# Optimization experiments

Measured on AMD Instinct MI355X. Metric: run time of the kernel, lower is better.

Reference implementation:

```python
import jax, jax.numpy as jnp
import numpy as np

B, N, X, Y, W1, W2, D = 2, 6, 8, 8, 8, 8, 128
H, DH = 4, 32
L = X * Y          # number of windows
QT = N * W1 * W2   # tokens per window
EPS = 1e-5


def _ln(x, g, b):
    m = x.mean(-1, keepdims=True)
    v = ((x - m) ** 2).mean(-1, keepdims=True)
    return (x - m) * jax.lax.rsqrt(v + EPS) * g + b


def _win(t):
    # b n x y w1 w2 d -> b (x y) (n w1 w2) d
    return t.transpose(0, 2, 3, 1, 4, 5, 6).reshape(B, L, QT, D)


def setup_inputs() -> dict:
    key = jax.random.key(0)
    ks = jax.random.split(key, 12)
    s = 0.02
    inp = {
        'q': jax.random.normal(ks[0], (B, N, X, Y, W1, W2, D), jnp.float32),
        'k': jax.random.normal(ks[1], (B, N, X, Y, W1, W2, D), jnp.float32),
        'v': jax.random.normal(ks[2], (B, N, X, Y, W1, W2, D), jnp.float32),
        'skip': jax.random.normal(ks[3], (B, X, Y, W1, W2, D), jnp.float32),
        'gq': jnp.ones((D,), jnp.float32), 'betq': jnp.zeros((D,), jnp.float32),
        'gk': jnp.ones((D,), jnp.float32), 'betk': jnp.zeros((D,), jnp.float32),
        'gv': jnp.ones((D,), jnp.float32), 'betv': jnp.zeros((D,), jnp.float32),
        'wq': jax.random.normal(ks[4], (D, H * DH), jnp.float32) * s,
        'bq': jnp.zeros((H * DH,), jnp.float32),
        'wk': jax.random.normal(ks[5], (D, H * DH), jnp.float32) * s,
        'bk': jnp.zeros((H * DH,), jnp.float32),
        'wv': jax.random.normal(ks[6], (D, H * DH), jnp.float32) * s,
        'bv': jnp.zeros((H * DH,), jnp.float32),
        'wp': jax.random.normal(ks[7], (H * DH, D), jnp.float32) * s,
        'bp': jnp.zeros((D,), jnp.float32),
    }
    return inp


def reference(q, k, v, skip, gq, betq, gk, betk, gv, betv,
              wq, bq, wk, bk, wv, bv, wp, bp):
    scale = DH ** -0.5
    qw, kw, vw = _win(q), _win(k), _win(v)
    # LayerNorm + Linear QKV, split heads: (b, l, T, h, dh)
    qh = (_ln(qw, gq, betq) @ wq + bq).reshape(B, L, QT, H, DH)
    kh = (_ln(kw, gk, betk) @ wk + bk).reshape(B, L, QT, H, DH)
    vh = (_ln(vw, gv, betv) @ wv + bv).reshape(B, L, QT, H, DH)
    dot = scale * jnp.einsum('blqhd,blkhd->bhlqk', qh, kh)
    att = jax.nn.softmax(dot, axis=-1)
    a = jnp.einsum('bhlqk,blkhd->blqhd', att, vh).reshape(B, L, QT, H * DH)
    # b (x y) (n w1 w2) d -> b n x y w1 w2 d
    a = a.reshape(B, X, Y, N, W1, W2, H * DH).transpose(0, 3, 1, 2, 4, 5, 6)
    z = a @ wp + bp
    z = z.mean(1)  # average over views
    return z + skip
```

## Files before the change

kernel.cpp:

```cpp
#include <hip/hip_runtime.h>


typedef unsigned short u16;
typedef __bf16 bf16x8 __attribute__((ext_vector_type(8)));
typedef float  f32x16 __attribute__((ext_vector_type(16)));
typedef unsigned short u16x8 __attribute__((ext_vector_type(8)));
typedef unsigned short u16x4 __attribute__((ext_vector_type(4)));

union U8 { u16x8 u; bf16x8 b; };

__device__ __forceinline__ u16 f2bf(float f){
  unsigned u = __float_as_uint(f);
  u += 0x7fffu + ((u >> 16) & 1u);
  return (u16)(u >> 16);
}

__device__ __forceinline__ f32x16 mfma_bf16(bf16x8 a, bf16x8 b, f32x16 c){
  return __builtin_amdgcn_mfma_f32_32x32x16_bf16(a, b, c, 0, 0, 0);
}


__global__ __launch_bounds__(128) void k_prep(
    const float* __restrict__ wq, const float* __restrict__ bq,
    const float* __restrict__ gq, const float* __restrict__ betq,
    const float* __restrict__ wk, const float* __restrict__ bk,
    const float* __restrict__ gk, const float* __restrict__ betk,
    const float* __restrict__ wv, const float* __restrict__ bv,
    const float* __restrict__ gv, const float* __restrict__ betv,
    const float* __restrict__ wp,
    u16* __restrict__ wqT, u16* __restrict__ wkT, u16* __restrict__ wvT, u16* __restrict__ wpT,
    float* __restrict__ bq2, float* __restrict__ bk2, float* __restrict__ bv2,
    float* __restrict__ uq2, float* __restrict__ uk2, float* __restrict__ uv2)
{
  const float ALPHA_Q = 0.17677669529663687f * 1.4426950408889634f;
  int wsel = blockIdx.x >> 2, qq = blockIdx.x & 3;
  int tid = threadIdx.x;
  const float *w, *bb, *g, *bet; u16* wT; float *b2, *u2; float alpha;
  if (wsel == 0){ w=wq; bb=bq; g=gq; bet=betq; wT=wqT; b2=bq2; u2=uq2; alpha=ALPHA_Q; }
  else if (wsel == 1){ w=wk; bb=bk; g=gk; bet=betk; wT=wkT; b2=bk2; u2=uk2; alpha=1.f; }
  else if (wsel == 2){ w=wv; bb=bv; g=gv; bet=betv; wT=wvT; b2=bv2; u2=uv2; alpha=1.f; }
  else { w=wp; bb=nullptr; g=nullptr; bet=nullptr; wT=wpT; b2=nullptr; u2=nullptr; alpha=1.f; }
  float sc = (g ? g[tid] : 1.f) * alpha;
  for (int nn = 0; nn < 32; nn++){
    int n = qq*32 + nn;
    wT[n*128 + tid] = f2bf(w[tid*128 + n] * sc);
  }
  if (qq == 0 && bb){
    float s = bb[tid], su = 0.f;
    for (int k2 = 0; k2 < 128; k2++){
      float wv_ = w[k2*128 + tid];
      s  += bet[k2] * wv_;
      su += g[k2] * wv_;
    }
    b2[tid] = s * alpha;
    u2[tid] = su * alpha;
  }
}

__global__ __launch_bounds__(256) void k_lnproj(
    const float* __restrict__ qg, const float* __restrict__ kg, const float* __restrict__ vg,
    const u16* __restrict__ wqT, const u16* __restrict__ wkT, const u16* __restrict__ wvT,
    const float* __restrict__ bq2, const float* __restrict__ bk2, const float* __restrict__ bv2,
    const float* __restrict__ uq2, const float* __restrict__ uk2, const float* __restrict__ uv2,
    u16* __restrict__ qh, u16* __restrict__ kh, u16* __restrict__ vh)
{
  __shared__ alignas(16) u16 Abf[64*136];
  __shared__ float s1s[64], s2s[64];
  int bid = blockIdx.x, tid = threadIdx.x;
  int which = bid % 3;
  int t = bid / 3;
  int n = t % 6, bl = t / 6;
  const float* src; const u16* wT; const float *b2, *u2; u16* dstb;
  if (which == 0){ src=qg; wT=wqT; b2=bq2; u2=uq2; dstb=qh; }
  else if (which == 1){ src=kg; wT=wkT; b2=bk2; u2=uk2; dstb=kh; }
  else { src=vg; wT=wvT; b2=bv2; u2=uv2; dstb=vh; }
  int b = bl >> 6, l = bl & 63;
  const float4* s4 = (const float4*)(src + (size_t)((b*6 + n)*64 + l)*64*128);
  #pragma unroll
  for (int i = 0; i < 8; i++){
    int idx = tid + i*256;
    int row = idx >> 5, c4 = idx & 31;
    float4 xv = s4[idx];
    float s1 = xv.x + xv.y + xv.z + xv.w;
    float s2 = xv.x*xv.x + xv.y*xv.y + xv.z*xv.z + xv.w*xv.w;
    #pragma unroll
    for (int m = 1; m < 32; m <<= 1){
      s1 += __shfl_xor(s1, m, 64);
      s2 += __shfl_xor(s2, m, 64);
    }
    if (c4 == 0){ s1s[row] = s1; s2s[row] = s2; }
    u16x4 pk = { f2bf(xv.x), f2bf(xv.y), f2bf(xv.z), f2bf(xv.w) };
    *(u16x4*)&Abf[row*136 + c4*4] = pk;
  }
  __syncthreads();
  if (tid < 64){
    float m = s1s[tid] * (1.f/128.f);
    float r = rsqrtf(s2s[tid] * (1.f/128.f) - m*m + 1e-5f);
    s1s[tid] = r;
    s2s[tid] = r * m;
  }
  int wave = tid >> 6, lane = tid & 63, lm = lane & 31, lh = lane >> 5;
  bf16x8 bfr[8];
  const u16* wrow = wT + (32*wave + lm)*128 + lh*8;
  #pragma unroll
  for (int ks = 0; ks < 8; ks++) bfr[ks] = *(const bf16x8*)(wrow + ks*16);
  f32x16 acc0, acc1;
  #pragma unroll
  for (int r = 0; r < 16; r++){ acc0[r]=0.f; acc1[r]=0.f; }
  #pragma unroll
  for (int ks = 0; ks < 8; ks++){
    bf16x8 a0 = *(const bf16x8*)&Abf[lm*136       + ks*16 + lh*8];
    bf16x8 a1 = *(const bf16x8*)&Abf[(32+lm)*136  + ks*16 + lh*8];
    acc0 = mfma_bf16(a0, bfr[ks], acc0);
    acc1 = mfma_bf16(a1, bfr[ks], acc1);
  }
  __syncthreads();
  int col = 32*wave + lm;
  float u2c = u2[col], bc = b2[col];
  u16* dst = dstb + ((size_t)(bl*4 + wave)*384 + n*64)*32 + lm;
  #pragma unroll
  for (int r = 0; r < 16; r++){
    int row0 = (r&3) + 8*(r>>2) + 4*lh;
    float y0 = s1s[row0]     * acc0[r] - s2s[row0]     * u2c + bc;
    float y1 = s1s[row0+32]  * acc1[r] - s2s[row0+32]  * u2c + bc;
    dst[(size_t)row0*32]      = f2bf(y0);
    dst[(size_t)(32+row0)*32] = f2bf(y1);
  }
}

__global__ __launch_bounds__(768, 6) void k_attn(
    const u16* __restrict__ qh, const u16* __restrict__ kh, const u16* __restrict__ vh,
    u16* __restrict__ abar)
{
  __shared__ alignas(16) u16 vts[32*408];
  __shared__ float abar_s[64*32];
  int bid = blockIdx.x, tid = threadIdx.x;
  int h = bid & 3, bl = bid >> 2;
  const u16* qb = qh + (size_t)bid * (384*32);
  const u16* kb = kh + (size_t)bid * (384*32);
  const u16* vb = vh + (size_t)bid * (384*32);

  #pragma unroll
  for (int i = 0; i < 2; i++){
    int c = tid + i*768;
    int key = c >> 2, part = c & 3;
    int u = key & 31, tt = key >> 5;
    int a = u >> 2;
    int anew = (a & 4) | ((a & 1) << 1) | ((a >> 1) & 1);
    int pos = tt*32 + anew*4 + (u & 3);
    u16x8 vv = *(const u16x8*)(vb + key*32 + part*8);
    #pragma unroll
    for (int j = 0; j < 8; j++) vts[(part*8 + j)*408 + pos] = vv[j];
  }
  for (int idx = tid; idx < 2048; idx += 768) abar_s[idx] = 0.f;
  __syncthreads();

  int wave = tid >> 6, lane = tid & 63, lm = lane & 31, lh = lane >> 5;
  int n = wave >> 1, qoff = (wave & 1) * 32;
  int qrow = n*64 + qoff + lm;

  bf16x8 qf0 = *(const bf16x8*)(qb + qrow*32 +      lh*8);
  bf16x8 qf1 = *(const bf16x8*)(qb + qrow*32 + 16 + lh*8);

  f32x16 oacc;
  #pragma unroll
  for (int r = 0; r < 16; r++) oacc[r] = 0.f;
  float sle = 0.f;

  const u16* vrow = &vts[lm*408 + 8*lh];

  for (int kt = 0; kt < 12; kt++){
    int K0 = kt*32;
    bf16x8 kf0 = *(const bf16x8*)(kb + (K0+lm)*32 +      lh*8);
    bf16x8 kf1 = *(const bf16x8*)(kb + (K0+lm)*32 + 16 + lh*8);
    f32x16 s;
    #pragma unroll
    for (int r = 0; r < 16; r++) s[r] = 0.f;
    s = mfma_bf16(kf0, qf0, s);
    s = mfma_bf16(kf1, qf1, s);
    U8 p0, p1;
    #pragma unroll
    for (int r = 0; r < 8; r++){
      float e0 = exp2f(s[r]);
      float e1 = exp2f(s[r+8]);
      sle += e0 + e1;
      p0.u[r] = f2bf(e0);
      p1.u[r] = f2bf(e1);
    }
    U8 vb0, vb1;
    vb0.u = *(const u16x8*)(vrow + K0);
    vb1.u = *(const u16x8*)(vrow + K0 + 16);
    oacc = mfma_bf16(p0.b, vb0.b, oacc);
    oacc = mfma_bf16(p1.b, vb1.b, oacc);
  }

  sle += __shfl_xor(sle, 32, 64);

  #pragma unroll
  for (int r = 0; r < 16; r++){
    int q_l = (r&3) + 8*(r>>2) + 4*lh;
    float norm = __shfl(sle, q_l, 64);
    float o = oacc[r] * ((1.f/6.f) / norm);
    atomicAdd(&abar_s[(qoff + q_l)*32 + lm], o);
  }
  __syncthreads();
  u16* ob = abar + (size_t)(bl*64)*128 + h*32;
  for (int idx = tid; idx < 2048; idx += 768){
    int w12 = idx >> 5, dh = idx & 31;
    ob[(size_t)w12*128 + dh] = f2bf(abar_s[idx]);
  }
}

__global__ __launch_bounds__(256) void k_out(
    const u16* __restrict__ abar, const u16* __restrict__ wpT,
    const float* __restrict__ bp, const float* __restrict__ skip,
    float* __restrict__ out)
{
  __shared__ alignas(16) u16 Als[64*136];
  int tid = threadIdx.x;
  int R0 = blockIdx.x * 64;
  #pragma unroll
  for (int i = 0; i < 4; i++){
    int c = tid + i*256;
    int row = c >> 4, part = c & 15;
    *(u16x8*)&Als[row*136 + part*8] = *(const u16x8*)(abar + (size_t)(R0+row)*128 + part*8);
  }
  __syncthreads();
  int wave = tid >> 6, lane = tid & 63, lm = lane & 31, lh = lane >> 5;
  bf16x8 bfr[8];
  const u16* wrow = wpT + (32*wave + lm)*128 + lh*8;
  #pragma unroll
  for (int ks = 0; ks < 8; ks++) bfr[ks] = *(const bf16x8*)(wrow + ks*16);
  f32x16 acc0, acc1;
  #pragma unroll
  for (int r = 0; r < 16; r++){ acc0[r]=0.f; acc1[r]=0.f; }
  #pragma unroll
  for (int ks = 0; ks < 8; ks++){
    bf16x8 a0 = *(const bf16x8*)&Als[lm*136      + ks*16 + lh*8];
    bf16x8 a1 = *(const bf16x8*)&Als[(32+lm)*136 + ks*16 + lh*8];
    acc0 = mfma_bf16(a0, bfr[ks], acc0);
    acc1 = mfma_bf16(a1, bfr[ks], acc1);
  }
  float bias = bp[32*wave + lm];
  #pragma unroll
  for (int r = 0; r < 16; r++){
    int row0 = (r&3) + 8*(r>>2) + 4*lh;
    size_t f0 = (size_t)(R0 + row0)*128 + 32*wave + lm;
    out[f0] = acc0[r] + bias + skip[f0];
    size_t f1 = (size_t)(R0 + 32 + row0)*128 + 32*wave + lm;
    out[f1] = acc1[r] + bias + skip[f1];
  }
}

extern "C" void kernel_launch(void* const* d_in, const int* in_sizes, int n_in,
                              void* d_out, int out_size, void* d_ws, size_t ws_size,
                              hipStream_t stream)
{
  const float* q    = (const float*)d_in[0];
  const float* k    = (const float*)d_in[1];
  const float* v    = (const float*)d_in[2];
  const float* skip = (const float*)d_in[3];
  const float* gq   = (const float*)d_in[4];
  const float* betq = (const float*)d_in[5];
  const float* gk   = (const float*)d_in[6];
  const float* betk = (const float*)d_in[7];
  const float* gv   = (const float*)d_in[8];
  const float* betv = (const float*)d_in[9];
  const float* wq   = (const float*)d_in[10];
  const float* bq   = (const float*)d_in[11];
  const float* wk   = (const float*)d_in[12];
  const float* bk   = (const float*)d_in[13];
  const float* wv   = (const float*)d_in[14];
  const float* bv   = (const float*)d_in[15];
  const float* wp   = (const float*)d_in[16];
  const float* bp   = (const float*)d_in[17];
  float* out = (float*)d_out;

  char* ws = (char*)d_ws;
  u16* wqT = (u16*)ws;
  u16* wkT = wqT + 16384;
  u16* wvT = wkT + 16384;
  u16* wpT = wvT + 16384;
  float* bq2 = (float*)(ws + 131072);
  float* bk2 = bq2 + 128;
  float* bv2 = bk2 + 128;
  float* uq2 = bv2 + 128;
  float* uk2 = uq2 + 128;
  float* uv2 = uk2 + 128;
  u16* qh = (u16*)(ws + 134144);
  u16* kh = qh + 6291456;
  u16* vh = kh + 6291456;
  u16* abar = vh + 6291456;

  k_prep  <<<16,   128, 0, stream>>>(wq,bq,gq,betq, wk,bk,gk,betk, wv,bv,gv,betv, wp,
                                     wqT,wkT,wvT,wpT, bq2,bk2,bv2, uq2,uk2,uv2);
  k_lnproj<<<2304, 256, 0, stream>>>(q,k,v, wqT,wkT,wvT, bq2,bk2,bv2, uq2,uk2,uv2, qh,kh,vh);
  k_attn  <<<512,  768, 0, stream>>>(qh,kh,vh, abar);
  k_out   <<<128,  256, 0, stream>>>(abar, wpT, bp, skip, out);
}
```

Baseline: 224.2 us.

## Use native bf16 conversion and raw exp2, rework weight prep through LDS

Replaces the hand-written float-to-bf16 rounding with native __bf16 casts, which can lower to hardware conversion instructions. Switches exp2f to the raw AMDGCN exp2 builtin. Computes the softmax reciprocal once per lane instead of dividing per output. Rewrites the weight-prep kernel to stage each weight matrix in LDS with coalesced float4 loads and a parallel reduction for the folded biases. The builtin exp2 drops range handling for denormals, and the native cast's rounding may differ slightly from the old helper.

```diff
diff --git a/kernel.cpp b/kernel.cpp
--- a/kernel.cpp
+++ b/kernel.cpp
@@ -3,24 +3,24 @@
 
 typedef unsigned short u16;
 typedef __bf16 bf16x8 __attribute__((ext_vector_type(8)));
+typedef __bf16 bf16x4 __attribute__((ext_vector_type(4)));
 typedef float  f32x16 __attribute__((ext_vector_type(16)));
 typedef unsigned short u16x8 __attribute__((ext_vector_type(8)));
-typedef unsigned short u16x4 __attribute__((ext_vector_type(4)));
 
 union U8 { u16x8 u; bf16x8 b; };
 
-__device__ __forceinline__ u16 f2bf(float f){
-  unsigned u = __float_as_uint(f);
-  u += 0x7fffu + ((u >> 16) & 1u);
-  return (u16)(u >> 16);
-}
+#if __has_builtin(__builtin_amdgcn_exp2f)
+#define EXP2(x) __builtin_amdgcn_exp2f(x)
+#else
+#define EXP2(x) exp2f(x)
+#endif
 
 __device__ __forceinline__ f32x16 mfma_bf16(bf16x8 a, bf16x8 b, f32x16 c){
   return __builtin_amdgcn_mfma_f32_32x32x16_bf16(a, b, c, 0, 0, 0);
 }
 
 
-__global__ __launch_bounds__(128) void k_prep(
+__global__ __launch_bounds__(512) void k_prep(
     const float* __restrict__ wq, const float* __restrict__ bq,
     const float* __restrict__ gq, const float* __restrict__ betq,
     const float* __restrict__ wk, const float* __restrict__ bk,
@@ -32,28 +32,55 @@
     float* __restrict__ bq2, float* __restrict__ bk2, float* __restrict__ bv2,
     float* __restrict__ uq2, float* __restrict__ uk2, float* __restrict__ uv2)
 {
+  __shared__ float wls[128*129];
+  __shared__ float gls[128], bls[128];
+  __shared__ float redb[512], redu[512];
   const float ALPHA_Q = 0.17677669529663687f * 1.4426950408889634f;
-  int wsel = blockIdx.x >> 2, qq = blockIdx.x & 3;
-  int tid = threadIdx.x;
+  int wsel = blockIdx.x, tid = threadIdx.x;
   const float *w, *bb, *g, *bet; u16* wT; float *b2, *u2; float alpha;
   if (wsel == 0){ w=wq; bb=bq; g=gq; bet=betq; wT=wqT; b2=bq2; u2=uq2; alpha=ALPHA_Q; }
   else if (wsel == 1){ w=wk; bb=bk; g=gk; bet=betk; wT=wkT; b2=bk2; u2=uk2; alpha=1.f; }
   else if (wsel == 2){ w=wv; bb=bv; g=gv; bet=betv; wT=wvT; b2=bv2; u2=uv2; alpha=1.f; }
   else { w=wp; bb=nullptr; g=nullptr; bet=nullptr; wT=wpT; b2=nullptr; u2=nullptr; alpha=1.f; }
-  float sc = (g ? g[tid] : 1.f) * alpha;
-  for (int nn = 0; nn < 32; nn++){
-    int n = qq*32 + nn;
-    wT[n*128 + tid] = f2bf(w[tid*128 + n] * sc);
-  }
-  if (qq == 0 && bb){
-    float s = bb[tid], su = 0.f;
-    for (int k2 = 0; k2 < 128; k2++){
-      float wv_ = w[k2*128 + tid];
-      s  += bet[k2] * wv_;
-      su += g[k2] * wv_;
-    }
-    b2[tid] = s * alpha;
-    u2[tid] = su * alpha;
+
+  if (tid < 128){
+    gls[tid] = g ? g[tid] : 1.f;
+    bls[tid] = bet ? bet[tid] : 0.f;
+  }
+  const float4* w4 = (const float4*)w;
+  #pragma unroll
+  for (int i = 0; i < 8; i++){
+    int idx = tid + i*512;
+    int row = idx >> 5, c4 = (idx & 31) * 4;
+    float4 x = w4[idx];
+    wls[row*129 + c4 + 0] = x.x;
+    wls[row*129 + c4 + 1] = x.y;
+    wls[row*129 + c4 + 2] = x.z;
+    wls[row*129 + c4 + 3] = x.w;
+  }
+  __syncthreads();
+  int n = tid >> 2, qp = tid & 3;
+  float sb = 0.f, su = 0.f;
+  alignas(16) __bf16 tmp[32];
+  #pragma unroll
+  for (int kk = 0; kk < 32; kk++){
+    int k2 = qp*32 + kk;
+    float wv_ = wls[k2*129 + n];
+    float gv_ = gls[k2];
+    sb += bls[k2] * wv_;
+    su += gv_ * wv_;
+    tmp[kk] = (__bf16)(wv_ * gv_ * alpha);
+  }
+  #pragma unroll
+  for (int j = 0; j < 4; j++)
+    *(bf16x8*)(wT + n*128 + qp*32 + j*8) = *(bf16x8*)&tmp[j*8];
+  redb[tid] = sb; redu[tid] = su;
+  __syncthreads();
+  if (qp == 0 && bb){
+    float s = bb[n] + redb[tid] + redb[tid+1] + redb[tid+2] + redb[tid+3];
+    float u = redu[tid] + redu[tid+1] + redu[tid+2] + redu[tid+3];
+    b2[n] = s * alpha;
+    u2[n] = u * alpha;
   }
 }
 
@@ -89,8 +116,10 @@
       s2 += __shfl_xor(s2, m, 64);
     }
     if (c4 == 0){ s1s[row] = s1; s2s[row] = s2; }
-    u16x4 pk = { f2bf(xv.x), f2bf(xv.y), f2bf(xv.z), f2bf(xv.w) };
-    *(u16x4*)&Abf[row*136 + c4*4] = pk;
+    bf16x4 pk;
+    pk[0] = (__bf16)xv.x; pk[1] = (__bf16)xv.y;
+    pk[2] = (__bf16)xv.z; pk[3] = (__bf16)xv.w;
+    *(bf16x4*)&Abf[row*136 + c4*4] = pk;
   }
   __syncthreads();
   if (tid < 64){
@@ -123,8 +152,8 @@
     int row0 = (r&3) + 8*(r>>2) + 4*lh;
     float y0 = s1s[row0]     * acc0[r] - s2s[row0]     * u2c + bc;
     float y1 = s1s[row0+32]  * acc1[r] - s2s[row0+32]  * u2c + bc;
-    dst[(size_t)row0*32]      = f2bf(y0);
-    dst[(size_t)(32+row0)*32] = f2bf(y1);
+    *(__bf16*)&dst[(size_t)row0*32]      = (__bf16)y0;
+    *(__bf16*)&dst[(size_t)(32+row0)*32] = (__bf16)y1;
   }
 }
 
@@ -181,11 +210,11 @@
     U8 p0, p1;
     #pragma unroll
     for (int r = 0; r < 8; r++){
-      float e0 = exp2f(s[r]);
-      float e1 = exp2f(s[r+8]);
+      float e0 = EXP2(s[r]);
+      float e1 = EXP2(s[r+8]);
       sle += e0 + e1;
-      p0.u[r] = f2bf(e0);
-      p1.u[r] = f2bf(e1);
+      p0.b[r] = (__bf16)e0;
+      p1.b[r] = (__bf16)e1;
     }
     U8 vb0, vb1;
     vb0.u = *(const u16x8*)(vrow + K0);
@@ -195,19 +224,19 @@
   }
 
   sle += __shfl_xor(sle, 32, 64);
+  float inv = (1.f/6.f) / sle;
 
   #pragma unroll
   for (int r = 0; r < 16; r++){
     int q_l = (r&3) + 8*(r>>2) + 4*lh;
-    float norm = __shfl(sle, q_l, 64);
-    float o = oacc[r] * ((1.f/6.f) / norm);
+    float o = oacc[r] * __shfl(inv, q_l, 64);
     atomicAdd(&abar_s[(qoff + q_l)*32 + lm], o);
   }
   __syncthreads();
   u16* ob = abar + (size_t)(bl*64)*128 + h*32;
   for (int idx = tid; idx < 2048; idx += 768){
     int w12 = idx >> 5, dh = idx & 31;
-    ob[(size_t)w12*128 + dh] = f2bf(abar_s[idx]);
+    *(__bf16*)&ob[(size_t)w12*128 + dh] = (__bf16)abar_s[idx];
   }
 }
 
@@ -292,7 +321,7 @@
   u16* vh = kh + 6291456;
   u16* abar = vh + 6291456;
 
-  k_prep  <<<16,   128, 0, stream>>>(wq,bq,gq,betq, wk,bk,gk,betk, wv,bv,gv,betv, wp,
+  k_prep  <<<4,    512, 0, stream>>>(wq,bq,gq,betq, wk,bk,gk,betk, wv,bv,gv,betv, wp,
                                      wqT,wkT,wvT,wpT, bq2,bk2,bv2, uq2,uk2,uv2);
   k_lnproj<<<2304, 256, 0, stream>>>(q,k,v, wqT,wkT,wvT, bq2,bk2,bv2, uq2,uk2,uv2, qh,kh,vh);
   k_attn  <<<512,  768, 0, stream>>>(qh,kh,vh, abar);
```

After: 221.4 us. No clear change (-1.2%).
